# Performance work log

Measured on AMD Instinct MI355X. Metric: run time of the kernel, lower is better.

Reference implementation:

```python
import jax, jax.numpy as jnp
import numpy as np

BATCH, FIELDS, DIM = 1024, 39, 32
L0_OUT, L1_OUT = 256, 128  # cin_layer_size


def setup_inputs() -> dict:
    key = jax.random.key(0)
    ks = jax.random.split(key, 5)
    x = jax.random.normal(ks[0], (BATCH, FIELDS, DIM), dtype=jnp.float32)
    # Conv1d(kernel_size=1) weights stored as (out_channels, in_channels)
    w0 = jax.random.normal(ks[1], (L0_OUT, FIELDS * FIELDS), dtype=jnp.float32) * 0.02
    b0 = jax.random.normal(ks[2], (L0_OUT,), dtype=jnp.float32) * 0.02
    w1 = jax.random.normal(ks[3], (L1_OUT, FIELDS * (L0_OUT // 2)), dtype=jnp.float32) * 0.02
    b1 = jax.random.normal(ks[4], (L1_OUT,), dtype=jnp.float32) * 0.02
    return {"x": x, "w0": w0, "b0": b0, "w1": w1, "b1": b1}


def _cin_layer(x0, h_prev, w, b):
    # outer product over field axes at each embedding position, then 1x1 conv (= GEMM over channels)
    bsz, m, d = x0.shape
    z = jnp.einsum('bmd,bnd->bmnd', x0, h_prev).reshape(bsz, m * h_prev.shape[1], d)
    return jax.nn.relu(jnp.einsum('bid,oi->bod', z, w) + b[None, :, None])


def reference(x, w0, b0, w1, b1):
    # Layer 0: cross x with itself -> (B, m*m, D) -> conv -> relu
    h0 = _cin_layer(x, x, w0, b0)            # (B, 256, D)
    h1a, h1b = jnp.split(h0, 2, axis=1)      # each (B, 128, D); h1a feeds next layer
    # Layer 1 (final): cross x with h1a
    h1 = _cin_layer(x, h1a, w1, b1)          # (B, 128, D)
    # sum-pool over embedding dim of concatenated hidden outputs (hidden_layer[1:])
    return jnp.sum(jnp.concatenate([h1b, h1], axis=1), axis=-1)  # (B, 256)
```

## Files before the change

kernel.cpp:

```cpp
#include <hip/hip_runtime.h>


typedef _Float16 f16x8 __attribute__((ext_vector_type(8)));
typedef float f32x4 __attribute__((ext_vector_type(4)));

#define NB 2
#define NBLK 512
#define THREADS 512
#define K0C 50
#define K0P 52
#define M1C 40
#define M1P 42

__global__ __launch_bounds__(256) void prep_kernel(
    const float* __restrict__ w0, const float* __restrict__ w1,
    _Float16* __restrict__ w0c, _Float16* __restrict__ w1c) {
  int stride = gridDim.x * blockDim.x;
  int tid = blockIdx.x * blockDim.x + threadIdx.x;
  const int n0 = K0P * 8192;
  for (int idx = tid; idx < n0; idx += stride) {
    int j = idx & 7, lhi = (idx >> 3) & 3, l15 = (idx >> 5) & 15;
    int mt = (idx >> 9) & 1, w8 = (idx >> 10) & 7, s = idx >> 13;
    int o = w8 * 32 + mt * 16 + l15;
    int ip = s * 32 + lhi * 8 + j;
    float v = 0.f;
    if (ip < 1560) {
      unsigned m = (unsigned)ip / 40u;
      unsigned n = (unsigned)ip - m * 40u;
      if (n < 39u) v = w0[o * 1521 + m * 39 + n];
    }
    w0c[idx] = (_Float16)v;
  }
  const int n1 = M1P * 16384;
  for (int idx = tid; idx < n1; idx += stride) {
    int j = idx & 7, lhi = (idx >> 3) & 3, l15 = (idx >> 5) & 15;
    int mt = (idx >> 9) & 1, kf = (idx >> 10) & 1, rt = (idx >> 11) & 3;
    int kh = (idx >> 13) & 1, m = idx >> 14;
    int o = rt * 32 + mt * 16 + l15;
    int k = kh * 64 + kf * 32 + lhi * 8 + j;
    float v = (m < 39) ? w1[o * 4992 + m * 128 + k] : 0.f;
    w1c[idx] = (_Float16)v;
  }
}

__global__ __launch_bounds__(512, 2) void cin_kernel(
    const float* __restrict__ x,
    const _Float16* __restrict__ w0c, const float* __restrict__ b0,
    const _Float16* __restrict__ w1c, const float* __restrict__ b1,
    float* __restrict__ out) {
  __shared__ __align__(16) _Float16 xs[NB * 32 * 40];
  __shared__ __align__(16) _Float16 h1[NB * 32 * 136];
  __shared__ __align__(16) float red[4 * 32 * 65];

  const int t = threadIdx.x;
  const int bb = blockIdx.x * NB;
  const int w = t >> 6;
  const int l15 = t & 15;
  const int lhi = (t >> 4) & 3;
  const int lane_off = ((l15 << 2) | lhi) << 3;

  for (int idx = t; idx < NB * 39 * 32; idx += THREADS) {
    int b = idx / 1248; int rem = idx - b * 1248;
    int m = rem >> 5; int d = rem & 31;
    xs[(b * 32 + d) * 40 + m] = (_Float16)x[(bb + b) * 1248 + rem];
  }
  if (t < NB * 32) xs[t * 40 + 39] = (_Float16)0.f;
  __syncthreads();

  f32x4 acc[2][4] = {};
  const _Float16* p0 = w0c + w * 1024 + lane_off;

  auto loadA0 = [&](int s, f16x8 (&af)[2]) {
    const _Float16* p = p0 + s * 8192;
    af[0] = *(const f16x8*)(p);
    af[1] = *(const f16x8*)(p + 512);
  };
  auto zfr = [&](int s, f16x8 (&bz)[4]) {
    unsigned i0 = (unsigned)(s * 32) + (unsigned)lhi * 8u;
    unsigned m = (i0 * 52429u) >> 21;
    unsigned nb = i0 - m * 40u;
#pragma unroll
    for (int nt = 0; nt < 4; ++nt) {
      int c = nt * 16 + l15;
      _Float16 xm = xs[c * 40 + m];
      f16x8 xn = *(const f16x8*)&xs[c * 40 + nb];
      bz[nt] = xn * xm;
    }
  };
  auto comp0 = [&](f16x8 (&af)[2], f16x8 (&bz)[4]) {
#pragma unroll
    for (int mt = 0; mt < 2; ++mt)
#pragma unroll
      for (int nt = 0; nt < 4; ++nt)
        acc[mt][nt] = __builtin_amdgcn_mfma_f32_16x16x32_f16(af[mt], bz[nt], acc[mt][nt], 0, 0, 0);
  };

  {
    f16x8 af0[2], af1[2], af2[2], af3[2];
    loadA0(0, af0); loadA0(1, af1); loadA0(2, af2); loadA0(3, af3);
    for (int s = 0; s < 48; s += 4) {
      f16x8 bz[4];
      zfr(s + 0, bz); comp0(af0, bz); loadA0(s + 4, af0);
      zfr(s + 1, bz); comp0(af1, bz); loadA0(s + 5, af1);
      zfr(s + 2, bz); comp0(af2, bz); loadA0(s + 6, af2);
      zfr(s + 3, bz); comp0(af3, bz); loadA0(s + 7, af3);
    }
    f16x8 bz[4];
    zfr(48, bz); comp0(af0, bz);
    zfr(49, bz); comp0(af1, bz);
  }

  if (w < 4) {
#pragma unroll
    for (int mt = 0; mt < 2; ++mt) {
#pragma unroll
      for (int nt = 0; nt < 4; ++nt) {
        int c = nt * 16 + l15;
        int hbase = c * 136;
#pragma unroll
        for (int r = 0; r < 4; ++r) {
          int o = w * 32 + mt * 16 + lhi * 4 + r;
          float v = fmaxf(acc[mt][nt][r] + b0[o], 0.f);
          h1[hbase + o] = (_Float16)v;
        }
      }
    }
  } else {
#pragma unroll
    for (int mt = 0; mt < 2; ++mt) {
#pragma unroll
      for (int r = 0; r < 4; ++r) {
        int o = w * 32 + mt * 16 + lhi * 4 + r;
        float bias = b0[o];
        float sb0 = 0.f, sb1 = 0.f;
#pragma unroll
        for (int nt = 0; nt < 4; ++nt) {
          float v = fmaxf(acc[mt][nt][r] + bias, 0.f);
          v += __shfl_xor(v, 1); v += __shfl_xor(v, 2);
          v += __shfl_xor(v, 4); v += __shfl_xor(v, 8);
          if (nt < 2) sb0 += v; else sb1 += v;
        }
        if (l15 == 0) {
          out[(bb + 0) * 256 + (o - 128)] = sb0;
          out[(bb + 1) * 256 + (o - 128)] = sb1;
        }
      }
    }
  }
  __syncthreads();

  const int rt = w >> 1;
  const int kh = w & 1;

  f16x8 hf[2][4];
#pragma unroll
  for (int kf = 0; kf < 2; ++kf)
#pragma unroll
    for (int nt = 0; nt < 4; ++nt)
      hf[kf][nt] = *(const f16x8*)&h1[(nt * 16 + l15) * 136 + (kh * 2 + kf) * 32 + lhi * 8];

  f32x4 acc2[2][4] = {};
  const _Float16* p1 = w1c + (kh * 4 + rt) * 2048 + lane_off;

  auto loadA1 = [&](int m, f16x8 (&wf)[2][2]) {
    const _Float16* p = p1 + m * 16384;
    wf[0][0] = *(const f16x8*)(p);
    wf[0][1] = *(const f16x8*)(p + 512);
    wf[1][0] = *(const f16x8*)(p + 1024);
    wf[1][1] = *(const f16x8*)(p + 1536);
  };
  auto computeM = [&](int m, f16x8 (&wf)[2][2]) {
    float xmv[4];
#pragma unroll
    for (int nt = 0; nt < 4; ++nt) xmv[nt] = (float)xs[(nt * 16 + l15) * 40 + m];
#pragma unroll
    for (int mt = 0; mt < 2; ++mt)
#pragma unroll
      for (int nt = 0; nt < 4; ++nt) {
        f32x4 Y = __builtin_amdgcn_mfma_f32_16x16x32_f16(wf[0][mt], hf[0][nt],
                                                         (f32x4){0.f, 0.f, 0.f, 0.f}, 0, 0, 0);
        Y = __builtin_amdgcn_mfma_f32_16x16x32_f16(wf[1][mt], hf[1][nt], Y, 0, 0, 0);
        acc2[mt][nt] += Y * xmv[nt];
      }
  };

  {
    f16x8 wfA[2][2], wfB[2][2];
    loadA1(0, wfA);
    loadA1(1, wfB);
    for (int m = 0; m < M1C; m += 2) {
      computeM(m, wfA);     loadA1(m + 2, wfA);
      computeM(m + 1, wfB); loadA1(m + 3, wfB);
    }
  }

  __syncthreads();
  if (kh == 1) {
#pragma unroll
    for (int mt = 0; mt < 2; ++mt)
#pragma unroll
      for (int nt = 0; nt < 4; ++nt)
#pragma unroll
        for (int r = 0; r < 4; ++r) {
          int row = mt * 16 + lhi * 4 + r, c = nt * 16 + l15;
          red[(rt * 32 + row) * 65 + c] = acc2[mt][nt][r];
        }
  }
  __syncthreads();
  if (kh == 0) {
#pragma unroll
    for (int mt = 0; mt < 2; ++mt)
#pragma unroll
      for (int nt = 0; nt < 4; ++nt)
#pragma unroll
        for (int r = 0; r < 4; ++r) {
          int row = mt * 16 + lhi * 4 + r, c = nt * 16 + l15;
          acc2[mt][nt][r] += red[(rt * 32 + row) * 65 + c];
        }

#pragma unroll
    for (int mt = 0; mt < 2; ++mt) {
#pragma unroll
      for (int r = 0; r < 4; ++r) {
        int o = rt * 32 + mt * 16 + lhi * 4 + r;
        float bias = b1[o];
        float sb0 = 0.f, sb1 = 0.f;
#pragma unroll
        for (int nt = 0; nt < 4; ++nt) {
          float v = fmaxf(acc2[mt][nt][r] + bias, 0.f);
          v += __shfl_xor(v, 1); v += __shfl_xor(v, 2);
          v += __shfl_xor(v, 4); v += __shfl_xor(v, 8);
          if (nt < 2) sb0 += v; else sb1 += v;
        }
        if (l15 == 0) {
          out[(bb + 0) * 256 + 128 + o] = sb0;
          out[(bb + 1) * 256 + 128 + o] = sb1;
        }
      }
    }
  }
}

extern "C" void kernel_launch(void* const* d_in, const int* in_sizes, int n_in,
                              void* d_out, int out_size, void* d_ws, size_t ws_size,
                              hipStream_t stream) {
  const float* x  = (const float*)d_in[0];
  const float* w0 = (const float*)d_in[1];
  const float* b0 = (const float*)d_in[2];
  const float* w1 = (const float*)d_in[3];
  const float* b1 = (const float*)d_in[4];
  float* out = (float*)d_out;

  _Float16* w0c = (_Float16*)d_ws;
  _Float16* w1c = w0c + K0P * 8192;

  prep_kernel<<<256, 256, 0, stream>>>(w0, w1, w0c, w1c);
  cin_kernel<<<NBLK, THREADS, 0, stream>>>(x, w0c, b0, w1c, b1, out);
}
```

Baseline: 84.03 us.

## Reorder layer-0 K index so B fragments reuse cached x chunks and prefetch LDS loads

The layer-0 reduction index is remapped so each 32-wide K step covers 4 m values times 8 contiguous n values, with n chunks shared across 10 steps. The kernel can then keep x[n] chunk vectors in registers and fetch only one scalar x[m] per step, where before it recomputed a divide and did a vector LDS load per step. The prep kernel repacks w0 to match, padding K to 1600 entries. LDS scalar loads for both layers are also software-prefetched one step ahead, at the cost of more registers and a fully unrolled 50-step loop.

```diff
diff --git a/kernel.cpp b/kernel.cpp
--- a/kernel.cpp
+++ b/kernel.cpp
@@ -7,7 +7,6 @@
 #define NB 2
 #define NBLK 512
 #define THREADS 512
-#define K0C 50
 #define K0P 52
 #define M1C 40
 #define M1P 42
@@ -24,10 +23,11 @@
     int o = w8 * 32 + mt * 16 + l15;
     int ip = s * 32 + lhi * 8 + j;
     float v = 0.f;
-    if (ip < 1560) {
-      unsigned m = (unsigned)ip / 40u;
-      unsigned n = (unsigned)ip - m * 40u;
-      if (n < 39u) v = w0[o * 1521 + m * 39 + n];
+    if (ip < 1600) {
+      int c5 = ip / 320;
+      int m = (ip - c5 * 320) >> 3;
+      int n = c5 * 8 + (ip & 7);
+      if (m < 39 && n < 39) v = w0[o * 1521 + m * 39 + n];
     }
     w0c[idx] = (_Float16)v;
   }
@@ -59,6 +59,10 @@
   const int lhi = (t >> 4) & 3;
   const int lane_off = ((l15 << 2) | lhi) << 3;
 
+  int xrow[4];
+#pragma unroll
+  for (int nt = 0; nt < 4; ++nt) xrow[nt] = (nt * 16 + l15) * 40;
+
   for (int idx = t; idx < NB * 39 * 32; idx += THREADS) {
     int b = idx / 1248; int rem = idx - b * 1248;
     int m = rem >> 5; int d = rem & 31;
@@ -70,44 +74,43 @@
   f32x4 acc[2][4] = {};
   const _Float16* p0 = w0c + w * 1024 + lane_off;
 
-  auto loadA0 = [&](int s, f16x8 (&af)[2]) {
+  f16x8 af[2][2];
+  f16x8 ck[2][4];
+  _Float16 xmr[2][4];
+
+  auto loadA0 = [&](int s, int b) {
     const _Float16* p = p0 + s * 8192;
-    af[0] = *(const f16x8*)(p);
-    af[1] = *(const f16x8*)(p + 512);
-  };
-  auto zfr = [&](int s, f16x8 (&bz)[4]) {
-    unsigned i0 = (unsigned)(s * 32) + (unsigned)lhi * 8u;
-    unsigned m = (i0 * 52429u) >> 21;
-    unsigned nb = i0 - m * 40u;
-#pragma unroll
-    for (int nt = 0; nt < 4; ++nt) {
-      int c = nt * 16 + l15;
-      _Float16 xm = xs[c * 40 + m];
-      f16x8 xn = *(const f16x8*)&xs[c * 40 + nb];
-      bz[nt] = xn * xm;
-    }
-  };
-  auto comp0 = [&](f16x8 (&af)[2], f16x8 (&bz)[4]) {
+    af[b][0] = *(const f16x8*)(p);
+    af[b][1] = *(const f16x8*)(p + 512);
+  };
+  auto loadCk = [&](int g, int b) {
+#pragma unroll
+    for (int nt = 0; nt < 4; ++nt)
+      ck[b][nt] = *(const f16x8*)&xs[xrow[nt] + g * 8];
+  };
+  auto xmld = [&](int s, int b) {
+    int m = 4 * (s % 10) + lhi;
+#pragma unroll
+    for (int nt = 0; nt < 4; ++nt) xmr[b][nt] = xs[xrow[nt] + m];
+  };
+
+  loadCk(0, 0);
+  xmld(0, 0);
+  loadA0(0, 0); loadA0(1, 1);
+#pragma unroll
+  for (int s = 0; s < 50; ++s) {
+    const int g = s / 10;
+    if (s + 1 < 50) xmld(s + 1, (s + 1) & 1);
+    if ((s % 10) == 0 && g + 1 < 5) loadCk(g + 1, (g + 1) & 1);
+    f16x8 bz[4];
+#pragma unroll
+    for (int nt = 0; nt < 4; ++nt) bz[nt] = ck[g & 1][nt] * xmr[s & 1][nt];
 #pragma unroll
     for (int mt = 0; mt < 2; ++mt)
 #pragma unroll
       for (int nt = 0; nt < 4; ++nt)
-        acc[mt][nt] = __builtin_amdgcn_mfma_f32_16x16x32_f16(af[mt], bz[nt], acc[mt][nt], 0, 0, 0);
-  };
-
-  {
-    f16x8 af0[2], af1[2], af2[2], af3[2];
-    loadA0(0, af0); loadA0(1, af1); loadA0(2, af2); loadA0(3, af3);
-    for (int s = 0; s < 48; s += 4) {
-      f16x8 bz[4];
-      zfr(s + 0, bz); comp0(af0, bz); loadA0(s + 4, af0);
-      zfr(s + 1, bz); comp0(af1, bz); loadA0(s + 5, af1);
-      zfr(s + 2, bz); comp0(af2, bz); loadA0(s + 6, af2);
-      zfr(s + 3, bz); comp0(af3, bz); loadA0(s + 7, af3);
-    }
-    f16x8 bz[4];
-    zfr(48, bz); comp0(af0, bz);
-    zfr(49, bz); comp0(af1, bz);
+        acc[mt][nt] = __builtin_amdgcn_mfma_f32_16x16x32_f16(af[s & 1][mt], bz[nt], acc[mt][nt], 0, 0, 0);
+    if (s + 2 <= 51) loadA0(s + 2, s & 1);
   }
 
   if (w < 4) {
@@ -162,6 +165,11 @@
   f32x4 acc2[2][4] = {};
   const _Float16* p1 = w1c + (kh * 4 + rt) * 2048 + lane_off;
 
+  float xmv[2][4];
+  auto xmvld = [&](int m, int b) {
+#pragma unroll
+    for (int nt = 0; nt < 4; ++nt) xmv[b][nt] = (float)xs[xrow[nt] + m];
+  };
   auto loadA1 = [&](int m, f16x8 (&wf)[2][2]) {
     const _Float16* p = p1 + m * 16384;
     wf[0][0] = *(const f16x8*)(p);
@@ -169,10 +177,7 @@
     wf[1][0] = *(const f16x8*)(p + 1024);
     wf[1][1] = *(const f16x8*)(p + 1536);
   };
-  auto computeM = [&](int m, f16x8 (&wf)[2][2]) {
-    float xmv[4];
-#pragma unroll
-    for (int nt = 0; nt < 4; ++nt) xmv[nt] = (float)xs[(nt * 16 + l15) * 40 + m];
+  auto computeM = [&](int m, f16x8 (&wf)[2][2], float (&xv)[4]) {
 #pragma unroll
     for (int mt = 0; mt < 2; ++mt)
 #pragma unroll
@@ -180,7 +185,7 @@
         f32x4 Y = __builtin_amdgcn_mfma_f32_16x16x32_f16(wf[0][mt], hf[0][nt],
                                                          (f32x4){0.f, 0.f, 0.f, 0.f}, 0, 0, 0);
         Y = __builtin_amdgcn_mfma_f32_16x16x32_f16(wf[1][mt], hf[1][nt], Y, 0, 0, 0);
-        acc2[mt][nt] += Y * xmv[nt];
+        acc2[mt][nt] += Y * xv[nt];
       }
   };
 
@@ -188,9 +193,12 @@
     f16x8 wfA[2][2], wfB[2][2];
     loadA1(0, wfA);
     loadA1(1, wfB);
+    xmvld(0, 0);
     for (int m = 0; m < M1C; m += 2) {
-      computeM(m, wfA);     loadA1(m + 2, wfA);
-      computeM(m + 1, wfB); loadA1(m + 3, wfB);
+      xmvld(m + 1, 1);
+      computeM(m, wfA, xmv[0]);     loadA1(m + 2, wfA);
+      if (m + 2 < M1C) xmvld(m + 2, 0);
+      computeM(m + 1, wfB, xmv[1]); loadA1(m + 3, wfB);
     }
   }
 
```

Measured after the change: 91.42 us. 8.8% more time.

## Process four batches per 1024-thread block and stagger layer-1 weight start per block

Applied to the files above, without the earlier changes.

Doubles the block size to 1024 threads handling four batch elements as two independent 8-wave families, halving the grid to 256 blocks so the same weight fragments are fetched by fewer blocks. Layer-1's loop over fields now starts at a per-block rotated offset so concurrent blocks read different weight slices, spreading L2/cache traffic. The xs-derived scale factors are prefetched one step ahead. The trade-off is one block per CU with a larger LDS footprint, which lowers latency hiding across blocks and leaves only 256 blocks for 256 CUs.

```diff
diff --git a/kernel.cpp b/kernel.cpp
--- a/kernel.cpp
+++ b/kernel.cpp
@@ -4,12 +4,10 @@
 typedef _Float16 f16x8 __attribute__((ext_vector_type(8)));
 typedef float f32x4 __attribute__((ext_vector_type(4)));
 
-#define NB 2
-#define NBLK 512
-#define THREADS 512
-#define K0C 50
+#define NB 4
+#define NBLK 256
+#define THREADS 1024
 #define K0P 52
-#define M1C 40
 #define M1P 42
 
 __global__ __launch_bounds__(256) void prep_kernel(
@@ -43,32 +41,38 @@
   }
 }
 
-__global__ __launch_bounds__(512, 2) void cin_kernel(
+__global__ __launch_bounds__(1024, 1) void cin_kernel(
     const float* __restrict__ x,
     const _Float16* __restrict__ w0c, const float* __restrict__ b0,
     const _Float16* __restrict__ w1c, const float* __restrict__ b1,
     float* __restrict__ out) {
-  __shared__ __align__(16) _Float16 xs[NB * 32 * 40];
-  __shared__ __align__(16) _Float16 h1[NB * 32 * 136];
-  __shared__ __align__(16) float red[4 * 32 * 65];
+  __shared__ __align__(16) _Float16 xs[128 * 40];
+  __shared__ __align__(16) _Float16 h1[2 * 64 * 136];
+  __shared__ __align__(16) float red[2 * 4 * 32 * 65];
 
   const int t = threadIdx.x;
   const int bb = blockIdx.x * NB;
   const int w = t >> 6;
+  const int fam = w >> 3;
+  const int w8 = w & 7;
   const int l15 = t & 15;
   const int lhi = (t >> 4) & 3;
   const int lane_off = ((l15 << 2) | lhi) << 3;
+
+  int xrow[4];
+#pragma unroll
+  for (int nt = 0; nt < 4; ++nt) xrow[nt] = (fam * 64 + nt * 16 + l15) * 40;
 
   for (int idx = t; idx < NB * 39 * 32; idx += THREADS) {
     int b = idx / 1248; int rem = idx - b * 1248;
     int m = rem >> 5; int d = rem & 31;
     xs[(b * 32 + d) * 40 + m] = (_Float16)x[(bb + b) * 1248 + rem];
   }
-  if (t < NB * 32) xs[t * 40 + 39] = (_Float16)0.f;
+  if (t < 128) xs[t * 40 + 39] = (_Float16)0.f;
   __syncthreads();
 
   f32x4 acc[2][4] = {};
-  const _Float16* p0 = w0c + w * 1024 + lane_off;
+  const _Float16* p0 = w0c + w8 * 1024 + lane_off;
 
   auto loadA0 = [&](int s, f16x8 (&af)[2]) {
     const _Float16* p = p0 + s * 8192;
@@ -81,9 +85,8 @@
     unsigned nb = i0 - m * 40u;
 #pragma unroll
     for (int nt = 0; nt < 4; ++nt) {
-      int c = nt * 16 + l15;
-      _Float16 xm = xs[c * 40 + m];
-      f16x8 xn = *(const f16x8*)&xs[c * 40 + nb];
+      _Float16 xm = xs[xrow[nt] + m];
+      f16x8 xn = *(const f16x8*)&xs[xrow[nt] + nb];
       bz[nt] = xn * xm;
     }
   };
@@ -110,16 +113,16 @@
     zfr(49, bz); comp0(af1, bz);
   }
 
-  if (w < 4) {
+  if (w8 < 4) {
 #pragma unroll
     for (int mt = 0; mt < 2; ++mt) {
 #pragma unroll
       for (int nt = 0; nt < 4; ++nt) {
         int c = nt * 16 + l15;
-        int hbase = c * 136;
+        int hbase = fam * 8704 + c * 136;
 #pragma unroll
         for (int r = 0; r < 4; ++r) {
-          int o = w * 32 + mt * 16 + lhi * 4 + r;
+          int o = w8 * 32 + mt * 16 + lhi * 4 + r;
           float v = fmaxf(acc[mt][nt][r] + b0[o], 0.f);
           h1[hbase + o] = (_Float16)v;
         }
@@ -130,7 +133,7 @@
     for (int mt = 0; mt < 2; ++mt) {
 #pragma unroll
       for (int r = 0; r < 4; ++r) {
-        int o = w * 32 + mt * 16 + lhi * 4 + r;
+        int o = w8 * 32 + mt * 16 + lhi * 4 + r;
         float bias = b0[o];
         float sb0 = 0.f, sb1 = 0.f;
 #pragma unroll
@@ -141,27 +144,32 @@
           if (nt < 2) sb0 += v; else sb1 += v;
         }
         if (l15 == 0) {
-          out[(bb + 0) * 256 + (o - 128)] = sb0;
-          out[(bb + 1) * 256 + (o - 128)] = sb1;
-        }
-      }
-    }
-  }
-  __syncthreads();
-
-  const int rt = w >> 1;
-  const int kh = w & 1;
+          out[(bb + fam * 2 + 0) * 256 + (o - 128)] = sb0;
+          out[(bb + fam * 2 + 1) * 256 + (o - 128)] = sb1;
+        }
+      }
+    }
+  }
+  __syncthreads();
+
+  const int rt = w8 >> 1;
+  const int kh = w8 & 1;
 
   f16x8 hf[2][4];
 #pragma unroll
   for (int kf = 0; kf < 2; ++kf)
 #pragma unroll
     for (int nt = 0; nt < 4; ++nt)
-      hf[kf][nt] = *(const f16x8*)&h1[(nt * 16 + l15) * 136 + (kh * 2 + kf) * 32 + lhi * 8];
+      hf[kf][nt] = *(const f16x8*)&h1[fam * 8704 + (nt * 16 + l15) * 136 + (kh * 2 + kf) * 32 + lhi * 8];
 
   f32x4 acc2[2][4] = {};
   const _Float16* p1 = w1c + (kh * 4 + rt) * 2048 + lane_off;
 
+  float xmv[2][4];
+  auto xmvld = [&](int m, int b) {
+#pragma unroll
+    for (int nt = 0; nt < 4; ++nt) xmv[b][nt] = (float)xs[xrow[nt] + m];
+  };
   auto loadA1 = [&](int m, f16x8 (&wf)[2][2]) {
     const _Float16* p = p1 + m * 16384;
     wf[0][0] = *(const f16x8*)(p);
@@ -169,10 +177,7 @@
     wf[1][0] = *(const f16x8*)(p + 1024);
     wf[1][1] = *(const f16x8*)(p + 1536);
   };
-  auto computeM = [&](int m, f16x8 (&wf)[2][2]) {
-    float xmv[4];
-#pragma unroll
-    for (int nt = 0; nt < 4; ++nt) xmv[nt] = (float)xs[(nt * 16 + l15) * 40 + m];
+  auto computeM = [&](f16x8 (&wf)[2][2], float (&xv)[4]) {
 #pragma unroll
     for (int mt = 0; mt < 2; ++mt)
 #pragma unroll
@@ -180,17 +185,27 @@
         f32x4 Y = __builtin_amdgcn_mfma_f32_16x16x32_f16(wf[0][mt], hf[0][nt],
                                                          (f32x4){0.f, 0.f, 0.f, 0.f}, 0, 0, 0);
         Y = __builtin_amdgcn_mfma_f32_16x16x32_f16(wf[1][mt], hf[1][nt], Y, 0, 0, 0);
-        acc2[mt][nt] += Y * xmv[nt];
+        acc2[mt][nt] += Y * xv[nt];
       }
   };
 
   {
+    int bph = ((blockIdx.x >> 3) & 7) * 5;
+    int me = bph;
+    int mo = bph + 1; if (mo >= 40) mo -= 40;
     f16x8 wfA[2][2], wfB[2][2];
-    loadA1(0, wfA);
-    loadA1(1, wfB);
-    for (int m = 0; m < M1C; m += 2) {
-      computeM(m, wfA);     loadA1(m + 2, wfA);
-      computeM(m + 1, wfB); loadA1(m + 3, wfB);
+    loadA1(me, wfA);
+    loadA1(mo, wfB);
+    xmvld(me, 0);
+    for (int it = 0; it < 20; ++it) {
+      xmvld(mo, 1);
+      computeM(wfA, xmv[0]);
+      me += 2; if (me >= 40) me -= 40;
+      loadA1(me, wfA);
+      if (it < 19) xmvld(me, 0);
+      computeM(wfB, xmv[1]);
+      mo += 2; if (mo >= 40) mo -= 40;
+      loadA1(mo, wfB);
     }
   }
 
@@ -203,7 +218,7 @@
 #pragma unroll
         for (int r = 0; r < 4; ++r) {
           int row = mt * 16 + lhi * 4 + r, c = nt * 16 + l15;
-          red[(rt * 32 + row) * 65 + c] = acc2[mt][nt][r];
+          red[fam * 8320 + (rt * 32 + row) * 65 + c] = acc2[mt][nt][r];
         }
   }
   __syncthreads();
@@ -215,7 +230,7 @@
 #pragma unroll
         for (int r = 0; r < 4; ++r) {
           int row = mt * 16 + lhi * 4 + r, c = nt * 16 + l15;
-          acc2[mt][nt][r] += red[(rt * 32 + row) * 65 + c];
+          acc2[mt][nt][r] += red[fam * 8320 + (rt * 32 + row) * 65 + c];
         }
 
 #pragma unroll
@@ -233,8 +248,8 @@
           if (nt < 2) sb0 += v; else sb1 += v;
         }
         if (l15 == 0) {
-          out[(bb + 0) * 256 + 128 + o] = sb0;
-          out[(bb + 1) * 256 + 128 + o] = sb1;
+          out[(bb + fam * 2 + 0) * 256 + 128 + o] = sb0;
+          out[(bb + fam * 2 + 1) * 256 + 128 + o] = sb1;
         }
       }
     }
```

Result: slower. 87.72 us (+4.4%).

## Split the two batch samples across two wave groups in 1024-thread blocks

Applied to the files above, without the earlier changes.

Doubles the block to 1024 threads and gives each group of 8 waves one of the two batch samples (32 columns), so every wave keeps half as many accumulators and B-fragments in both GEMM stages. The layer-1 cross-wave reduction buffer is resized per group, and the reduction is folded into the bias/ReLU/pool epilogue. This is meant to raise wave-level parallelism and latency hiding per CU. In exchange, each weight fragment is reused across fewer columns, so both groups load the same A-fragments and global/L2 weight traffic per block doubles.

```diff
diff --git a/kernel.cpp b/kernel.cpp
--- a/kernel.cpp
+++ b/kernel.cpp
@@ -6,10 +6,8 @@
 
 #define NB 2
 #define NBLK 512
-#define THREADS 512
-#define K0C 50
+#define THREADS 1024
 #define K0P 52
-#define M1C 40
 #define M1P 42
 
 __global__ __launch_bounds__(256) void prep_kernel(
@@ -43,21 +41,27 @@
   }
 }
 
-__global__ __launch_bounds__(512, 2) void cin_kernel(
+__global__ __launch_bounds__(1024, 8) void cin_kernel(
     const float* __restrict__ x,
     const _Float16* __restrict__ w0c, const float* __restrict__ b0,
     const _Float16* __restrict__ w1c, const float* __restrict__ b1,
     float* __restrict__ out) {
   __shared__ __align__(16) _Float16 xs[NB * 32 * 40];
   __shared__ __align__(16) _Float16 h1[NB * 32 * 136];
-  __shared__ __align__(16) float red[4 * 32 * 65];
+  __shared__ __align__(16) float red[8 * 32 * 34];
 
   const int t = threadIdx.x;
   const int bb = blockIdx.x * NB;
   const int w = t >> 6;
+  const int fam = w >> 3;
+  const int w8 = w & 7;
   const int l15 = t & 15;
   const int lhi = (t >> 4) & 3;
   const int lane_off = ((l15 << 2) | lhi) << 3;
+
+  int xrow[2];
+#pragma unroll
+  for (int nt = 0; nt < 2; ++nt) xrow[nt] = (fam * 32 + nt * 16 + l15) * 40;
 
   for (int idx = t; idx < NB * 39 * 32; idx += THREADS) {
     int b = idx / 1248; int rem = idx - b * 1248;
@@ -67,31 +71,30 @@
   if (t < NB * 32) xs[t * 40 + 39] = (_Float16)0.f;
   __syncthreads();
 
-  f32x4 acc[2][4] = {};
-  const _Float16* p0 = w0c + w * 1024 + lane_off;
+  f32x4 acc[2][2] = {};
+  const _Float16* p0 = w0c + w8 * 1024 + lane_off;
 
   auto loadA0 = [&](int s, f16x8 (&af)[2]) {
     const _Float16* p = p0 + s * 8192;
     af[0] = *(const f16x8*)(p);
     af[1] = *(const f16x8*)(p + 512);
   };
-  auto zfr = [&](int s, f16x8 (&bz)[4]) {
+  auto zfr = [&](int s, f16x8 (&bz)[2]) {
     unsigned i0 = (unsigned)(s * 32) + (unsigned)lhi * 8u;
     unsigned m = (i0 * 52429u) >> 21;
     unsigned nb = i0 - m * 40u;
 #pragma unroll
-    for (int nt = 0; nt < 4; ++nt) {
-      int c = nt * 16 + l15;
-      _Float16 xm = xs[c * 40 + m];
-      f16x8 xn = *(const f16x8*)&xs[c * 40 + nb];
+    for (int nt = 0; nt < 2; ++nt) {
+      _Float16 xm = xs[xrow[nt] + m];
+      f16x8 xn = *(const f16x8*)&xs[xrow[nt] + nb];
       bz[nt] = xn * xm;
     }
   };
-  auto comp0 = [&](f16x8 (&af)[2], f16x8 (&bz)[4]) {
-#pragma unroll
-    for (int mt = 0; mt < 2; ++mt)
-#pragma unroll
-      for (int nt = 0; nt < 4; ++nt)
+  auto comp0 = [&](f16x8 (&af)[2], f16x8 (&bz)[2]) {
+#pragma unroll
+    for (int mt = 0; mt < 2; ++mt)
+#pragma unroll
+      for (int nt = 0; nt < 2; ++nt)
         acc[mt][nt] = __builtin_amdgcn_mfma_f32_16x16x32_f16(af[mt], bz[nt], acc[mt][nt], 0, 0, 0);
   };
 
@@ -99,67 +102,56 @@
     f16x8 af0[2], af1[2], af2[2], af3[2];
     loadA0(0, af0); loadA0(1, af1); loadA0(2, af2); loadA0(3, af3);
     for (int s = 0; s < 48; s += 4) {
-      f16x8 bz[4];
+      f16x8 bz[2];
       zfr(s + 0, bz); comp0(af0, bz); loadA0(s + 4, af0);
       zfr(s + 1, bz); comp0(af1, bz); loadA0(s + 5, af1);
       zfr(s + 2, bz); comp0(af2, bz); loadA0(s + 6, af2);
       zfr(s + 3, bz); comp0(af3, bz); loadA0(s + 7, af3);
     }
-    f16x8 bz[4];
+    f16x8 bz[2];
     zfr(48, bz); comp0(af0, bz);
     zfr(49, bz); comp0(af1, bz);
   }
 
-  if (w < 4) {
-#pragma unroll
-    for (int mt = 0; mt < 2; ++mt) {
-#pragma unroll
-      for (int nt = 0; nt < 4; ++nt) {
-        int c = nt * 16 + l15;
-        int hbase = c * 136;
+  if (w8 < 4) {
+#pragma unroll
+    for (int mt = 0; mt < 2; ++mt)
+#pragma unroll
+      for (int nt = 0; nt < 2; ++nt) {
+        int c = fam * 32 + nt * 16 + l15;
 #pragma unroll
         for (int r = 0; r < 4; ++r) {
-          int o = w * 32 + mt * 16 + lhi * 4 + r;
+          int o = w8 * 32 + mt * 16 + lhi * 4 + r;
           float v = fmaxf(acc[mt][nt][r] + b0[o], 0.f);
-          h1[hbase + o] = (_Float16)v;
+          h1[c * 136 + o] = (_Float16)v;
         }
       }
-    }
   } else {
 #pragma unroll
-    for (int mt = 0; mt < 2; ++mt) {
+    for (int mt = 0; mt < 2; ++mt)
 #pragma unroll
       for (int r = 0; r < 4; ++r) {
-        int o = w * 32 + mt * 16 + lhi * 4 + r;
+        int o = w8 * 32 + mt * 16 + lhi * 4 + r;
         float bias = b0[o];
-        float sb0 = 0.f, sb1 = 0.f;
-#pragma unroll
-        for (int nt = 0; nt < 4; ++nt) {
-          float v = fmaxf(acc[mt][nt][r] + bias, 0.f);
-          v += __shfl_xor(v, 1); v += __shfl_xor(v, 2);
-          v += __shfl_xor(v, 4); v += __shfl_xor(v, 8);
-          if (nt < 2) sb0 += v; else sb1 += v;
-        }
-        if (l15 == 0) {
-          out[(bb + 0) * 256 + (o - 128)] = sb0;
-          out[(bb + 1) * 256 + (o - 128)] = sb1;
-        }
-      }
-    }
-  }
-  __syncthreads();
-
-  const int rt = w >> 1;
-  const int kh = w & 1;
-
-  f16x8 hf[2][4];
+        float v = fmaxf(acc[mt][0][r] + bias, 0.f) + fmaxf(acc[mt][1][r] + bias, 0.f);
+        v += __shfl_xor(v, 1); v += __shfl_xor(v, 2);
+        v += __shfl_xor(v, 4); v += __shfl_xor(v, 8);
+        if (l15 == 0) out[(bb + fam) * 256 + (o - 128)] = v;
+      }
+  }
+  __syncthreads();
+
+  const int rt = w8 >> 1;
+  const int kh = w8 & 1;
+
+  f16x8 hf[2][2];
 #pragma unroll
   for (int kf = 0; kf < 2; ++kf)
 #pragma unroll
-    for (int nt = 0; nt < 4; ++nt)
-      hf[kf][nt] = *(const f16x8*)&h1[(nt * 16 + l15) * 136 + (kh * 2 + kf) * 32 + lhi * 8];
-
-  f32x4 acc2[2][4] = {};
+    for (int nt = 0; nt < 2; ++nt)
+      hf[kf][nt] = *(const f16x8*)&h1[(fam * 32 + nt * 16 + l15) * 136 + kh * 64 + kf * 32 + lhi * 8];
+
+  f32x4 acc2[2][2] = {};
   const _Float16* p1 = w1c + (kh * 4 + rt) * 2048 + lane_off;
 
   auto loadA1 = [&](int m, f16x8 (&wf)[2][2]) {
@@ -170,13 +162,13 @@
     wf[1][1] = *(const f16x8*)(p + 1536);
   };
   auto computeM = [&](int m, f16x8 (&wf)[2][2]) {
-    float xmv[4];
-#pragma unroll
-    for (int nt = 0; nt < 4; ++nt) xmv[nt] = (float)xs[(nt * 16 + l15) * 40 + m];
-#pragma unroll
-    for (int mt = 0; mt < 2; ++mt)
-#pragma unroll
-      for (int nt = 0; nt < 4; ++nt) {
+    float xmv[2];
+#pragma unroll
+    for (int nt = 0; nt < 2; ++nt) xmv[nt] = (float)xs[xrow[nt] + m];
+#pragma unroll
+    for (int mt = 0; mt < 2; ++mt)
+#pragma unroll
+      for (int nt = 0; nt < 2; ++nt) {
         f32x4 Y = __builtin_amdgcn_mfma_f32_16x16x32_f16(wf[0][mt], hf[0][nt],
                                                          (f32x4){0.f, 0.f, 0.f, 0.f}, 0, 0, 0);
         Y = __builtin_amdgcn_mfma_f32_16x16x32_f16(wf[1][mt], hf[1][nt], Y, 0, 0, 0);
@@ -188,7 +180,7 @@
     f16x8 wfA[2][2], wfB[2][2];
     loadA1(0, wfA);
     loadA1(1, wfB);
-    for (int m = 0; m < M1C; m += 2) {
+    for (int m = 0; m < 40; m += 2) {
       computeM(m, wfA);     loadA1(m + 2, wfA);
       computeM(m + 1, wfB); loadA1(m + 3, wfB);
     }
@@ -199,43 +191,31 @@
 #pragma unroll
     for (int mt = 0; mt < 2; ++mt)
 #pragma unroll
-      for (int nt = 0; nt < 4; ++nt)
+      for (int nt = 0; nt < 2; ++nt)
 #pragma unroll
         for (int r = 0; r < 4; ++r) {
           int row = mt * 16 + lhi * 4 + r, c = nt * 16 + l15;
-          red[(rt * 32 + row) * 65 + c] = acc2[mt][nt][r];
+          red[(fam * 4 + rt) * 1088 + row * 34 + c] = acc2[mt][nt][r];
         }
   }
   __syncthreads();
   if (kh == 0) {
-#pragma unroll
-    for (int mt = 0; mt < 2; ++mt)
-#pragma unroll
-      for (int nt = 0; nt < 4; ++nt)
-#pragma unroll
-        for (int r = 0; r < 4; ++r) {
-          int row = mt * 16 + lhi * 4 + r, c = nt * 16 + l15;
-          acc2[mt][nt][r] += red[(rt * 32 + row) * 65 + c];
-        }
-
 #pragma unroll
     for (int mt = 0; mt < 2; ++mt) {
 #pragma unroll
       for (int r = 0; r < 4; ++r) {
         int o = rt * 32 + mt * 16 + lhi * 4 + r;
         float bias = b1[o];
-        float sb0 = 0.f, sb1 = 0.f;
-#pragma unroll
-        for (int nt = 0; nt < 4; ++nt) {
-          float v = fmaxf(acc2[mt][nt][r] + bias, 0.f);
-          v += __shfl_xor(v, 1); v += __shfl_xor(v, 2);
-          v += __shfl_xor(v, 4); v += __shfl_xor(v, 8);
-          if (nt < 2) sb0 += v; else sb1 += v;
+        int row = mt * 16 + lhi * 4 + r;
+        float v = 0.f;
+#pragma unroll
+        for (int nt = 0; nt < 2; ++nt) {
+          float tot = acc2[mt][nt][r] + red[(fam * 4 + rt) * 1088 + row * 34 + nt * 16 + l15];
+          v += fmaxf(tot + bias, 0.f);
         }
-        if (l15 == 0) {
-          out[(bb + 0) * 256 + 128 + o] = sb0;
-          out[(bb + 1) * 256 + 128 + o] = sb1;
-        }
+        v += __shfl_xor(v, 1); v += __shfl_xor(v, 2);
+        v += __shfl_xor(v, 4); v += __shfl_xor(v, 8);
+        if (l15 == 0) out[(bb + fam) * 256 + 128 + o] = v;
       }
     }
   }
```

New measurement: 291.2 us. +246.5%, slower.
